# Kernel optimization log

Measured on AMD Instinct MI355X. Metric: run time of the kernel, lower is better.

## Reference

```python
import jax, jax.numpy as jnp
import numpy as np

B, A, N, K, F, E = 2, 5, 1000, 16, 256, 3


def setup_inputs() -> dict:
    key = jax.random.key(0)
    ks = jax.random.split(key, 6)
    nfeature = jax.random.normal(ks[0], (B, A, N, F), dtype=jnp.float32)
    nn_idx = jax.random.randint(ks[1], (B, A, N, K), 0, N)
    etype = jax.random.randint(ks[2], (B, A, N, K), 0, E)
    W = jax.random.normal(ks[3], (A, E, F, F), dtype=jnp.float32) * (1.0 / np.sqrt(F))
    b = jnp.zeros((A, E, F), dtype=jnp.float32)
    W1 = jax.random.normal(ks[4], (A, F, F), dtype=jnp.float32) * (1.0 / np.sqrt(F))
    W2 = jax.random.normal(ks[5], (A, F, F), dtype=jnp.float32) * (1.0 / np.sqrt(F))
    b2 = jnp.zeros((A, F), dtype=jnp.float32)
    return {"nfeature": nfeature, "nn_idx": nn_idx, "etype": etype,
            "W": W, "b": b, "W1": W1, "W2": W2, "b2": b2}


def reference(nfeature, nn_idx, etype, W, b, W1, W2, b2):
    Bs, As, Ns, Fs = nfeature.shape
    Ks = nn_idx.shape[-1]
    Es = W.shape[1]
    # gather neighbor features per anchor: [B, A, N, K, F]
    idx = nn_idx.reshape(Bs, As, Ns * Ks, 1)
    nbr = jnp.take_along_axis(nfeature, idx, axis=2).reshape(Bs, As, Ns, Ks, Fs)
    onehot = jax.nn.one_hot(etype, Es, dtype=nfeature.dtype)  # [B, A, N, K, E]
    # edge-type-specific pointwise transform (loop over small fixed E)
    msg = jnp.zeros((Bs, As, Ns, Ks, Fs), dtype=nfeature.dtype)
    for e in range(Es):
        y = jnp.einsum('bankf,afg->bankg', nbr, W[:, e]) + b[:, e][None, :, None, None, :]
        msg = msg + onehot[..., e:e + 1] * y
    pw = jax.nn.relu(msg.mean(axis=3))  # aggregate over K neighbors -> [B, A, N, F]
    # hop: mix each anchor with the summed 'mutual' feature
    mutual = pw.sum(axis=1)  # [B, N, F]
    hop = jax.nn.relu(jnp.einsum('banf,afg->bang', pw, W1)
                      + jnp.einsum('bnf,afg->bang', mutual, W2)
                      + b2[None, :, None, :])
    return hop + nfeature  # residual add
```

## Files before the change

### kernel.cpp

```cpp
#include <hip/hip_runtime.h>

typedef float f32x4 __attribute__((ext_vector_type(4)));
typedef __bf16 bf16x8 __attribute__((ext_vector_type(8)));
typedef unsigned short u16x4 __attribute__((ext_vector_type(4)));
typedef unsigned short u16x8 __attribute__((ext_vector_type(8)));

constexpr int B_ = 2, A_ = 5, N_ = 1000, K_ = 16, F_ = 256, E_ = 3;
constexpr int RTOT = B_ * N_;
constexpr int ROWS = 2016;
constexpr int TIL  = 32;
constexpr int NT   = ROWS / TIL;
constexpr int GBL  = NT * A_;
constexpr int KS1  = (E_ * F_) / 32;
constexpr int KS2  = (2 * F_) / 32;
constexpr int NTL  = F_ / 16;

constexpr int GATHER_BLOCKS = (A_ * ROWS) / 4;
constexpr int PACK_THREADS  = A_ * KS1 * NTL * 64 + A_ * KS2 * NTL * 64;
constexpr int PACK_BLOCKS   = PACK_THREADS / 256;

constexpr size_t SZ_WPK  = (size_t)A_ * KS1 * NTL * 512 * 2;
constexpr size_t OFF_W12 = SZ_WPK;
constexpr size_t SZ_W12  = (size_t)A_ * KS2 * NTL * 512 * 2;
constexpr size_t OFF_PWB = OFF_W12 + SZ_W12;
constexpr size_t SZ_PWB  = (size_t)A_ * ROWS * F_ * 2;
constexpr size_t OFF_SG  = OFF_PWB + SZ_PWB;
constexpr size_t SZ_SG   = (size_t)A_ * ROWS * (E_ * F_) * 2;
constexpr size_t OFF_CNT = OFF_SG + SZ_SG;

__device__ __forceinline__ unsigned short f2bf(float x) {
  unsigned int u = __builtin_bit_cast(unsigned int, x);
  u += 0x7fffu + ((u >> 16) & 1u);
  return (unsigned short)(u >> 16);
}
__device__ __forceinline__ float bf2f(unsigned short h) {
  return __builtin_bit_cast(float, (unsigned int)h << 16);
}
__device__ __forceinline__ int swz315(int bid) {
  const int xcd = bid & 7, idx = bid >> 3;
  return (xcd < 3 ? xcd * 40 : 120 + (xcd - 3) * 39) + idx;
}

__global__ __launch_bounds__(256) void k_gather_pack(
    const float* __restrict__ nf, const int* __restrict__ nn_idx,
    const int* __restrict__ et, const float* __restrict__ W,
    const float* __restrict__ W1, const float* __restrict__ W2,
    unsigned short* __restrict__ Sg, float* __restrict__ CNTS,
    unsigned short* __restrict__ wpk, unsigned short* __restrict__ w12)
{
  if (blockIdx.x < GATHER_BLOCKS) {
    const int bid  = blockIdx.x;
    const int nbid = (bid & 7) * (GATHER_BLOCKS / 8) + (bid >> 3);
    const int task = nbid * 4 + (threadIdx.x >> 6);
    const int lane = threadIdx.x & 63;
    const int a  = task / ROWS;
    const int rp = task - a * ROWS;
    const int rg = rp < RTOT ? rp : RTOT - 1;
    const int bb = rg / N_;
    const int n  = rg - bb * N_;
    const int eoff = ((bb * A_ + a) * N_ + n) * K_;

    int4 iv[4], ev[4];
#pragma unroll
    for (int q = 0; q < 4; ++q) {
      iv[q] = *reinterpret_cast<const int4*>(nn_idx + eoff + q * 4);
      ev[q] = *reinterpret_cast<const int4*>(et + eoff + q * 4);
    }
    const float* __restrict__ slab =
        nf + (size_t)(bb * A_ + a) * N_ * F_ + lane * 4;
    f32x4 a0 = {0.f, 0.f, 0.f, 0.f}, a1 = a0, a2 = a0;
    int c0 = 0, c1 = 0, c2 = 0;
#pragma unroll
    for (int q = 0; q < 4; ++q) {
#pragma unroll
      for (int j = 0; j < 4; ++j) {
        const int id = ((const int*)&iv[q])[j];
        const int e  = ((const int*)&ev[q])[j];
        const f32x4 v = *reinterpret_cast<const f32x4*>(slab + (size_t)id * F_);
        if (e == 0)      { a0 += v; ++c0; }
        else if (e == 1) { a1 += v; ++c1; }
        else             { a2 += v; ++c2; }
      }
    }
    unsigned short* __restrict__ row = Sg + ((size_t)a * ROWS + rp) * 768;
    const int sw = (rp & 7) << 3;
    u16x4 p0, p1, p2;
#pragma unroll
    for (int j = 0; j < 4; ++j) {
      p0[j] = f2bf(a0[j]); p1[j] = f2bf(a1[j]); p2[j] = f2bf(a2[j]);
    }
    *reinterpret_cast<u16x4*>(row + ((0 * F_ + lane * 4) ^ sw)) = p0;
    *reinterpret_cast<u16x4*>(row + ((1 * F_ + lane * 4) ^ sw)) = p1;
    *reinterpret_cast<u16x4*>(row + ((2 * F_ + lane * 4) ^ sw)) = p2;
    if (lane == 0) {
      f32x4 c = {(float)c0, (float)c1, (float)c2, 0.f};
      *reinterpret_cast<f32x4*>(CNTS + (size_t)task * 4) = c;
    }
  } else {
    const int id = (blockIdx.x - GATHER_BLOCKS) * 256 + threadIdx.x;
    const int T1 = A_ * KS1 * NTL * 64;
    const int T2 = A_ * KS2 * NTL * 64;
    if (id < T1) {
      const int lane = id & 63, nt = (id >> 6) & 15;
      const int r = id >> 10, t = r % KS1, a = r / KS1;
      const int k0 = t * 32 + (lane >> 4) * 8;
      const int n  = nt * 16 + (lane & 15);
      const float* src = W + ((size_t)a * E_ * F_ + k0) * F_ + n;
      u16x8 v;
#pragma unroll
      for (int j = 0; j < 8; ++j) v[j] = f2bf(src[(size_t)j * F_]);
      *reinterpret_cast<u16x8*>(wpk + (size_t)id * 8) = v;
    } else if (id < T1 + T2) {
      const int p = id - T1;
      const int lane = p & 63, nt = (p >> 6) & 15;
      const int r = p >> 10, t = r % KS2, a = r / KS2;
      const int k0 = t * 32 + (lane >> 4) * 8;
      const int n  = nt * 16 + (lane & 15);
      u16x8 v;
#pragma unroll
      for (int j = 0; j < 8; ++j) {
        const int k = k0 + j;
        const float s = (k < F_) ? W1[((size_t)a * F_ + k) * F_ + n]
                                 : W2[((size_t)a * F_ + (k - F_)) * F_ + n];
        v[j] = f2bf(s);
      }
      *reinterpret_cast<u16x8*>(w12 + (size_t)p * 8) = v;
    }
  }
}

__global__ __launch_bounds__(512) void k_gemm1(
    const unsigned short* __restrict__ Sg, const float* __restrict__ CNTS,
    const unsigned short* __restrict__ wpk, const float* __restrict__ bias,
    unsigned short* __restrict__ pwb)
{
  __shared__ alignas(16) unsigned short S[TIL * E_ * F_];
  __shared__ float CNT[TIL][4];
  const int lin = swz315(blockIdx.x);
  const int a   = lin / NT;
  const int r0  = (lin - a * NT) * TIL;
  const int tid = threadIdx.x;

  const unsigned short* src = Sg + ((size_t)a * ROWS + r0) * 768;
#pragma unroll
  for (int it = 0; it < 6; ++it) {
    const int off = (it * 512 + tid) * 8;
    __builtin_amdgcn_global_load_lds(
        (const __attribute__((address_space(1))) unsigned int*)(src + off),
        (__attribute__((address_space(3))) unsigned int*)(S + off), 16, 0, 0);
  }
  if (tid < TIL)
    *reinterpret_cast<f32x4*>(&CNT[tid][0]) =
        *reinterpret_cast<const f32x4*>(CNTS + (size_t)(a * ROWS + r0 + tid) * 4);
  __syncthreads();

  const int lane = tid & 63, wv = tid >> 6;
  const int arow = lane & 15, kg = lane >> 4;
  const unsigned short* __restrict__ Wp = wpk + (size_t)a * KS1 * NTL * 512;
  f32x4 acc[2][2];
#pragma unroll
  for (int c = 0; c < 2; ++c)
#pragma unroll
    for (int mb = 0; mb < 2; ++mb) acc[c][mb] = (f32x4){0.f, 0.f, 0.f, 0.f};
  const int ssw = (arow & 7) << 3;
#pragma unroll
  for (int t = 0; t < KS1; ++t) {
    bf16x8 af[2];
#pragma unroll
    for (int mb = 0; mb < 2; ++mb) {
      const int si = ((mb * 16 + arow) * 768 + t * 32 + kg * 8) ^ ssw;
      af[mb] = *reinterpret_cast<const bf16x8*>(&S[si]);
    }
#pragma unroll
    for (int c = 0; c < 2; ++c) {
      const int nt = wv * 2 + c;
      const bf16x8 bfr = *reinterpret_cast<const bf16x8*>(
          Wp + ((size_t)(t * NTL + nt) * 64 + lane) * 8);
#pragma unroll
      for (int mb = 0; mb < 2; ++mb)
        acc[c][mb] = __builtin_amdgcn_mfma_f32_16x16x32_bf16(af[mb], bfr, acc[c][mb], 0, 0, 0);
    }
  }

  const float* __restrict__ ba = bias + a * E_ * F_;
#pragma unroll
  for (int c = 0; c < 2; ++c) {
    const int col = (wv * 2 + c) * 16 + arow;
    const float b0 = ba[col], b1 = ba[F_ + col], b2v = ba[2 * F_ + col];
#pragma unroll
    for (int mb = 0; mb < 2; ++mb) {
#pragma unroll
      for (int rr = 0; rr < 4; ++rr) {
        const int row = mb * 16 + kg * 4 + rr;
        const int r   = r0 + row;
        float x = (acc[c][mb][rr] + CNT[row][0] * b0 + CNT[row][1] * b1 +
                   CNT[row][2] * b2v) * (1.0f / K_);
        x = fmaxf(x, 0.f);
        pwb[((size_t)a * ROWS + r) * F_ + (col ^ ((row & 7) << 3))] = f2bf(x);
      }
    }
  }
}

__global__ __launch_bounds__(512) void k_hop_mfma(
    const unsigned short* __restrict__ pwb, const unsigned short* __restrict__ w12,
    const float* __restrict__ b2, const float* __restrict__ nf,
    float* __restrict__ out)
{
  __shared__ alignas(16) unsigned short S2[2 * TIL * F_];
  const int lin = swz315(blockIdx.x);
  const int a   = lin / NT;
  const int r0  = (lin - a * NT) * TIL;
  const int tid = threadIdx.x;

  const unsigned short* srcP = pwb + ((size_t)a * ROWS + r0) * F_;
#pragma unroll
  for (int it = 0; it < 2; ++it) {
    const int off = (it * 512 + tid) * 8;
    __builtin_amdgcn_global_load_lds(
        (const __attribute__((address_space(1))) unsigned int*)(srcP + off),
        (__attribute__((address_space(3))) unsigned int*)(S2 + off), 16, 0, 0);
  }
#pragma unroll
  for (int it = 0; it < 2; ++it) {
    const int i = (it * 512 + tid) * 8;
    float s[8] = {0.f, 0.f, 0.f, 0.f, 0.f, 0.f, 0.f, 0.f};
#pragma unroll
    for (int a2 = 0; a2 < A_; ++a2) {
      const u16x8 v = *reinterpret_cast<const u16x8*>(
          pwb + ((size_t)a2 * ROWS + r0) * F_ + i);
#pragma unroll
      for (int j = 0; j < 8; ++j) s[j] += bf2f(v[j]);
    }
    u16x8 o;
#pragma unroll
    for (int j = 0; j < 8; ++j) o[j] = f2bf(s[j]);
    *reinterpret_cast<u16x8*>(&S2[TIL * F_ + i]) = o;
  }
  __syncthreads();

  const int lane = tid & 63, wv = tid >> 6;
  const int arow = lane & 15, kg = lane >> 4;
  const unsigned short* __restrict__ Wp = w12 + (size_t)a * KS2 * NTL * 512;
  f32x4 acc[2][2];
#pragma unroll
  for (int c = 0; c < 2; ++c)
#pragma unroll
    for (int mb = 0; mb < 2; ++mb) acc[c][mb] = (f32x4){0.f, 0.f, 0.f, 0.f};
  const int ssw = (arow & 7) << 3;
#pragma unroll
  for (int t = 0; t < KS2; ++t) {
    const int half = t >> 3;
    const int kk   = (t & 7) * 32;
    bf16x8 af[2];
#pragma unroll
    for (int mb = 0; mb < 2; ++mb) {
      const int si = half * (TIL * F_) + (mb * 16 + arow) * F_ + ((kk + kg * 8) ^ ssw);
      af[mb] = *reinterpret_cast<const bf16x8*>(&S2[si]);
    }
#pragma unroll
    for (int c = 0; c < 2; ++c) {
      const int nt = wv * 2 + c;
      const bf16x8 bfr = *reinterpret_cast<const bf16x8*>(
          Wp + ((size_t)(t * NTL + nt) * 64 + lane) * 8);
#pragma unroll
      for (int mb = 0; mb < 2; ++mb)
        acc[c][mb] = __builtin_amdgcn_mfma_f32_16x16x32_bf16(af[mb], bfr, acc[c][mb], 0, 0, 0);
    }
  }

#pragma unroll
  for (int c = 0; c < 2; ++c) {
    const int col = (wv * 2 + c) * 16 + arow;
    const float bb2 = b2[a * F_ + col];
#pragma unroll
    for (int mb = 0; mb < 2; ++mb) {
#pragma unroll
      for (int rr = 0; rr < 4; ++rr) {
        const int row = mb * 16 + kg * 4 + rr;
        const int r   = r0 + row;
        if (r < RTOT) {
          const int bb = r / N_, n = r - bb * N_;
          const size_t o = ((size_t)(bb * A_ + a) * N_ + n) * F_ + col;
          out[o] = fmaxf(acc[c][mb][rr] + bb2, 0.f) + nf[o];
        }
      }
    }
  }
}

extern "C" void kernel_launch(void* const* d_in, const int* in_sizes, int n_in,
                              void* d_out, int out_size, void* d_ws, size_t ws_size,
                              hipStream_t stream)
{
  const float* nf     = (const float*)d_in[0];
  const int*   nn_idx = (const int*)  d_in[1];
  const int*   et     = (const int*)  d_in[2];
  const float* W      = (const float*)d_in[3];
  const float* bias   = (const float*)d_in[4];
  const float* W1     = (const float*)d_in[5];
  const float* W2     = (const float*)d_in[6];
  const float* b2     = (const float*)d_in[7];
  float* out = (float*)d_out;

  unsigned short* wpk  = (unsigned short*)d_ws;
  unsigned short* w12  = (unsigned short*)((char*)d_ws + OFF_W12);
  unsigned short* pwb  = (unsigned short*)((char*)d_ws + OFF_PWB);
  unsigned short* Sg   = (unsigned short*)((char*)d_ws + OFF_SG);
  float*          CNTS = (float*)((char*)d_ws + OFF_CNT);

  k_gather_pack<<<dim3(GATHER_BLOCKS + PACK_BLOCKS), 256, 0, stream>>>(
      nf, nn_idx, et, W, W1, W2, Sg, CNTS, wpk, w12);

  k_gemm1<<<dim3(GBL), 512, 0, stream>>>(Sg, CNTS, wpk, bias, pwb);
  k_hop_mfma<<<dim3(GBL), 512, 0, stream>>>(pwb, w12, b2, nf, out);
}
```

Before: 47.97 us.

## Fuse neighbor gather into first GEMM via shared memory, split weight packing

The gather-and-bucket step now writes its per-edge-type sums straight into shared memory inside the first GEMM kernel, using 16-row tiles of 256 threads. This removes the global round trip of the bf16 gathered buffer and the count buffer. Weight packing moves into its own small kernel that runs before the fused kernel, which now waits for it. The risks are less reuse of each weight fragment per block, because tiles are smaller, and a serial pack launch on the critical path.

```diff
diff --git a/kernel.cpp b/kernel.cpp
--- a/kernel.cpp
+++ b/kernel.cpp
@@ -8,25 +8,24 @@
 constexpr int B_ = 2, A_ = 5, N_ = 1000, K_ = 16, F_ = 256, E_ = 3;
 constexpr int RTOT = B_ * N_;
 constexpr int ROWS = 2016;
-constexpr int TIL  = 32;
-constexpr int NT   = ROWS / TIL;
-constexpr int GBL  = NT * A_;
+constexpr int TILE = 16;
+constexpr int NT1  = RTOT / TILE;
+constexpr int GBL1 = NT1 * A_;
+constexpr int TIL2 = 32;
+constexpr int NT2  = ROWS / TIL2;
+constexpr int GBL2 = NT2 * A_;
 constexpr int KS1  = (E_ * F_) / 32;
 constexpr int KS2  = (2 * F_) / 32;
 constexpr int NTL  = F_ / 16;
 
-constexpr int GATHER_BLOCKS = (A_ * ROWS) / 4;
-constexpr int PACK_THREADS  = A_ * KS1 * NTL * 64 + A_ * KS2 * NTL * 64;
-constexpr int PACK_BLOCKS   = PACK_THREADS / 256;
+constexpr int PACK_THREADS = A_ * KS1 * NTL * 64 + A_ * KS2 * NTL * 64;
+constexpr int PACK_BLOCKS  = PACK_THREADS / 256;
 
 constexpr size_t SZ_WPK  = (size_t)A_ * KS1 * NTL * 512 * 2;
 constexpr size_t OFF_W12 = SZ_WPK;
 constexpr size_t SZ_W12  = (size_t)A_ * KS2 * NTL * 512 * 2;
 constexpr size_t OFF_PWB = OFF_W12 + SZ_W12;
 constexpr size_t SZ_PWB  = (size_t)A_ * ROWS * F_ * 2;
-constexpr size_t OFF_SG  = OFF_PWB + SZ_PWB;
-constexpr size_t SZ_SG   = (size_t)A_ * ROWS * (E_ * F_) * 2;
-constexpr size_t OFF_CNT = OFF_SG + SZ_SG;
 
 __device__ __forceinline__ unsigned short f2bf(float x) {
   unsigned int u = __builtin_bit_cast(unsigned int, x);
@@ -36,30 +35,70 @@
 __device__ __forceinline__ float bf2f(unsigned short h) {
   return __builtin_bit_cast(float, (unsigned int)h << 16);
 }
+__device__ __forceinline__ int swz625(int bid) {
+  const int xcd = bid & 7, idx = bid >> 3;
+  return (xcd == 0 ? 0 : 79 + (xcd - 1) * 78) + idx;
+}
 __device__ __forceinline__ int swz315(int bid) {
   const int xcd = bid & 7, idx = bid >> 3;
   return (xcd < 3 ? xcd * 40 : 120 + (xcd - 3) * 39) + idx;
 }
 
-__global__ __launch_bounds__(256) void k_gather_pack(
+__global__ __launch_bounds__(256) void k_pack(
+    const float* __restrict__ W, const float* __restrict__ W1,
+    const float* __restrict__ W2, unsigned short* __restrict__ wpk,
+    unsigned short* __restrict__ w12)
+{
+  const int id = blockIdx.x * 256 + threadIdx.x;
+  const int T1 = A_ * KS1 * NTL * 64;
+  const int T2 = A_ * KS2 * NTL * 64;
+  if (id < T1) {
+    const int lane = id & 63, nt = (id >> 6) & 15;
+    const int r = id >> 10, t = r % KS1, a = r / KS1;
+    const int k0 = t * 32 + (lane >> 4) * 8;
+    const int n  = nt * 16 + (lane & 15);
+    const float* src = W + ((size_t)a * E_ * F_ + k0) * F_ + n;
+    u16x8 v;
+#pragma unroll
+    for (int j = 0; j < 8; ++j) v[j] = f2bf(src[(size_t)j * F_]);
+    *reinterpret_cast<u16x8*>(wpk + (size_t)id * 8) = v;
+  } else if (id < T1 + T2) {
+    const int p = id - T1;
+    const int lane = p & 63, nt = (p >> 6) & 15;
+    const int r = p >> 10, t = r % KS2, a = r / KS2;
+    const int k0 = t * 32 + (lane >> 4) * 8;
+    const int n  = nt * 16 + (lane & 15);
+    u16x8 v;
+#pragma unroll
+    for (int j = 0; j < 8; ++j) {
+      const int k = k0 + j;
+      const float s = (k < F_) ? W1[((size_t)a * F_ + k) * F_ + n]
+                               : W2[((size_t)a * F_ + (k - F_)) * F_ + n];
+      v[j] = f2bf(s);
+    }
+    *reinterpret_cast<u16x8*>(w12 + (size_t)p * 8) = v;
+  }
+}
+
+__global__ __launch_bounds__(256) void k_fused(
     const float* __restrict__ nf, const int* __restrict__ nn_idx,
-    const int* __restrict__ et, const float* __restrict__ W,
-    const float* __restrict__ W1, const float* __restrict__ W2,
-    unsigned short* __restrict__ Sg, float* __restrict__ CNTS,
-    unsigned short* __restrict__ wpk, unsigned short* __restrict__ w12)
-{
-  if (blockIdx.x < GATHER_BLOCKS) {
-    const int bid  = blockIdx.x;
-    const int nbid = (bid & 7) * (GATHER_BLOCKS / 8) + (bid >> 3);
-    const int task = nbid * 4 + (threadIdx.x >> 6);
-    const int lane = threadIdx.x & 63;
-    const int a  = task / ROWS;
-    const int rp = task - a * ROWS;
-    const int rg = rp < RTOT ? rp : RTOT - 1;
-    const int bb = rg / N_;
-    const int n  = rg - bb * N_;
+    const int* __restrict__ et, const unsigned short* __restrict__ wpk,
+    const float* __restrict__ bias, unsigned short* __restrict__ pwb)
+{
+  __shared__ alignas(16) unsigned short S[TILE * E_ * F_];
+  __shared__ float CNT[TILE][4];
+  const int lin = swz625(blockIdx.x);
+  const int a   = lin / NT1;
+  const int r0  = (lin - a * NT1) * TILE;
+  const int tid = threadIdx.x;
+  const int lane = tid & 63, wv = tid >> 6;
+
+#pragma unroll
+  for (int rr = 0; rr < 4; ++rr) {
+    const int row = wv * 4 + rr;
+    const int r   = r0 + row;
+    const int bb  = r / N_, n = r - bb * N_;
     const int eoff = ((bb * A_ + a) * N_ + n) * K_;
-
     int4 iv[4], ev[4];
 #pragma unroll
     for (int q = 0; q < 4; ++q) {
@@ -82,122 +121,53 @@
         else             { a2 += v; ++c2; }
       }
     }
-    unsigned short* __restrict__ row = Sg + ((size_t)a * ROWS + rp) * 768;
-    const int sw = (rp & 7) << 3;
+    const int sw = (row & 7) << 3;
     u16x4 p0, p1, p2;
 #pragma unroll
     for (int j = 0; j < 4; ++j) {
       p0[j] = f2bf(a0[j]); p1[j] = f2bf(a1[j]); p2[j] = f2bf(a2[j]);
     }
-    *reinterpret_cast<u16x4*>(row + ((0 * F_ + lane * 4) ^ sw)) = p0;
-    *reinterpret_cast<u16x4*>(row + ((1 * F_ + lane * 4) ^ sw)) = p1;
-    *reinterpret_cast<u16x4*>(row + ((2 * F_ + lane * 4) ^ sw)) = p2;
+    *reinterpret_cast<u16x4*>(&S[(row * 768 + 0 * F_ + lane * 4) ^ sw]) = p0;
+    *reinterpret_cast<u16x4*>(&S[(row * 768 + 1 * F_ + lane * 4) ^ sw]) = p1;
+    *reinterpret_cast<u16x4*>(&S[(row * 768 + 2 * F_ + lane * 4) ^ sw]) = p2;
     if (lane == 0) {
-      f32x4 c = {(float)c0, (float)c1, (float)c2, 0.f};
-      *reinterpret_cast<f32x4*>(CNTS + (size_t)task * 4) = c;
-    }
-  } else {
-    const int id = (blockIdx.x - GATHER_BLOCKS) * 256 + threadIdx.x;
-    const int T1 = A_ * KS1 * NTL * 64;
-    const int T2 = A_ * KS2 * NTL * 64;
-    if (id < T1) {
-      const int lane = id & 63, nt = (id >> 6) & 15;
-      const int r = id >> 10, t = r % KS1, a = r / KS1;
-      const int k0 = t * 32 + (lane >> 4) * 8;
-      const int n  = nt * 16 + (lane & 15);
-      const float* src = W + ((size_t)a * E_ * F_ + k0) * F_ + n;
-      u16x8 v;
-#pragma unroll
-      for (int j = 0; j < 8; ++j) v[j] = f2bf(src[(size_t)j * F_]);
-      *reinterpret_cast<u16x8*>(wpk + (size_t)id * 8) = v;
-    } else if (id < T1 + T2) {
-      const int p = id - T1;
-      const int lane = p & 63, nt = (p >> 6) & 15;
-      const int r = p >> 10, t = r % KS2, a = r / KS2;
-      const int k0 = t * 32 + (lane >> 4) * 8;
-      const int n  = nt * 16 + (lane & 15);
-      u16x8 v;
-#pragma unroll
-      for (int j = 0; j < 8; ++j) {
-        const int k = k0 + j;
-        const float s = (k < F_) ? W1[((size_t)a * F_ + k) * F_ + n]
-                                 : W2[((size_t)a * F_ + (k - F_)) * F_ + n];
-        v[j] = f2bf(s);
-      }
-      *reinterpret_cast<u16x8*>(w12 + (size_t)p * 8) = v;
-    }
-  }
-}
-
-__global__ __launch_bounds__(512) void k_gemm1(
-    const unsigned short* __restrict__ Sg, const float* __restrict__ CNTS,
-    const unsigned short* __restrict__ wpk, const float* __restrict__ bias,
-    unsigned short* __restrict__ pwb)
-{
-  __shared__ alignas(16) unsigned short S[TIL * E_ * F_];
-  __shared__ float CNT[TIL][4];
-  const int lin = swz315(blockIdx.x);
-  const int a   = lin / NT;
-  const int r0  = (lin - a * NT) * TIL;
-  const int tid = threadIdx.x;
-
-  const unsigned short* src = Sg + ((size_t)a * ROWS + r0) * 768;
-#pragma unroll
-  for (int it = 0; it < 6; ++it) {
-    const int off = (it * 512 + tid) * 8;
-    __builtin_amdgcn_global_load_lds(
-        (const __attribute__((address_space(1))) unsigned int*)(src + off),
-        (__attribute__((address_space(3))) unsigned int*)(S + off), 16, 0, 0);
-  }
-  if (tid < TIL)
-    *reinterpret_cast<f32x4*>(&CNT[tid][0]) =
-        *reinterpret_cast<const f32x4*>(CNTS + (size_t)(a * ROWS + r0 + tid) * 4);
+      CNT[row][0] = (float)c0; CNT[row][1] = (float)c1; CNT[row][2] = (float)c2;
+    }
+  }
   __syncthreads();
 
-  const int lane = tid & 63, wv = tid >> 6;
   const int arow = lane & 15, kg = lane >> 4;
   const unsigned short* __restrict__ Wp = wpk + (size_t)a * KS1 * NTL * 512;
-  f32x4 acc[2][2];
-#pragma unroll
-  for (int c = 0; c < 2; ++c)
-#pragma unroll
-    for (int mb = 0; mb < 2; ++mb) acc[c][mb] = (f32x4){0.f, 0.f, 0.f, 0.f};
+  f32x4 acc[4];
+#pragma unroll
+  for (int m = 0; m < 4; ++m) acc[m] = (f32x4){0.f, 0.f, 0.f, 0.f};
   const int ssw = (arow & 7) << 3;
 #pragma unroll
   for (int t = 0; t < KS1; ++t) {
-    bf16x8 af[2];
-#pragma unroll
-    for (int mb = 0; mb < 2; ++mb) {
-      const int si = ((mb * 16 + arow) * 768 + t * 32 + kg * 8) ^ ssw;
-      af[mb] = *reinterpret_cast<const bf16x8*>(&S[si]);
-    }
-#pragma unroll
-    for (int c = 0; c < 2; ++c) {
-      const int nt = wv * 2 + c;
+    const int si = (arow * 768 + t * 32 + kg * 8) ^ ssw;
+    const bf16x8 af = *reinterpret_cast<const bf16x8*>(&S[si]);
+#pragma unroll
+    for (int m = 0; m < 4; ++m) {
+      const int nt = wv * 4 + m;
       const bf16x8 bfr = *reinterpret_cast<const bf16x8*>(
           Wp + ((size_t)(t * NTL + nt) * 64 + lane) * 8);
-#pragma unroll
-      for (int mb = 0; mb < 2; ++mb)
-        acc[c][mb] = __builtin_amdgcn_mfma_f32_16x16x32_bf16(af[mb], bfr, acc[c][mb], 0, 0, 0);
+      acc[m] = __builtin_amdgcn_mfma_f32_16x16x32_bf16(af, bfr, acc[m], 0, 0, 0);
     }
   }
 
   const float* __restrict__ ba = bias + a * E_ * F_;
 #pragma unroll
-  for (int c = 0; c < 2; ++c) {
-    const int col = (wv * 2 + c) * 16 + arow;
+  for (int m = 0; m < 4; ++m) {
+    const int col = (wv * 4 + m) * 16 + arow;
     const float b0 = ba[col], b1 = ba[F_ + col], b2v = ba[2 * F_ + col];
 #pragma unroll
-    for (int mb = 0; mb < 2; ++mb) {
-#pragma unroll
-      for (int rr = 0; rr < 4; ++rr) {
-        const int row = mb * 16 + kg * 4 + rr;
-        const int r   = r0 + row;
-        float x = (acc[c][mb][rr] + CNT[row][0] * b0 + CNT[row][1] * b1 +
-                   CNT[row][2] * b2v) * (1.0f / K_);
-        x = fmaxf(x, 0.f);
-        pwb[((size_t)a * ROWS + r) * F_ + (col ^ ((row & 7) << 3))] = f2bf(x);
-      }
+    for (int rr = 0; rr < 4; ++rr) {
+      const int row = kg * 4 + rr;
+      const int r   = r0 + row;
+      float x = (acc[m][rr] + CNT[row][0] * b0 + CNT[row][1] * b1 +
+                 CNT[row][2] * b2v) * (1.0f / K_);
+      x = fmaxf(x, 0.f);
+      pwb[((size_t)a * ROWS + r) * F_ + (col ^ ((row & 7) << 3))] = f2bf(x);
     }
   }
 }
@@ -207,10 +177,10 @@
     const float* __restrict__ b2, const float* __restrict__ nf,
     float* __restrict__ out)
 {
-  __shared__ alignas(16) unsigned short S2[2 * TIL * F_];
+  __shared__ alignas(16) unsigned short S2[2 * TIL2 * F_];
   const int lin = swz315(blockIdx.x);
-  const int a   = lin / NT;
-  const int r0  = (lin - a * NT) * TIL;
+  const int a   = lin / NT2;
+  const int r0  = (lin - a * NT2) * TIL2;
   const int tid = threadIdx.x;
 
   const unsigned short* srcP = pwb + ((size_t)a * ROWS + r0) * F_;
@@ -235,7 +205,7 @@
     u16x8 o;
 #pragma unroll
     for (int j = 0; j < 8; ++j) o[j] = f2bf(s[j]);
-    *reinterpret_cast<u16x8*>(&S2[TIL * F_ + i]) = o;
+    *reinterpret_cast<u16x8*>(&S2[TIL2 * F_ + i]) = o;
   }
   __syncthreads();
 
@@ -255,7 +225,7 @@
     bf16x8 af[2];
 #pragma unroll
     for (int mb = 0; mb < 2; ++mb) {
-      const int si = half * (TIL * F_) + (mb * 16 + arow) * F_ + ((kk + kg * 8) ^ ssw);
+      const int si = half * (TIL2 * F_) + (mb * 16 + arow) * F_ + ((kk + kg * 8) ^ ssw);
       af[mb] = *reinterpret_cast<const bf16x8*>(&S2[si]);
     }
 #pragma unroll
@@ -303,15 +273,11 @@
   const float* b2     = (const float*)d_in[7];
   float* out = (float*)d_out;
 
-  unsigned short* wpk  = (unsigned short*)d_ws;
-  unsigned short* w12  = (unsigned short*)((char*)d_ws + OFF_W12);
-  unsigned short* pwb  = (unsigned short*)((char*)d_ws + OFF_PWB);
-  unsigned short* Sg   = (unsigned short*)((char*)d_ws + OFF_SG);
-  float*          CNTS = (float*)((char*)d_ws + OFF_CNT);
-
-  k_gather_pack<<<dim3(GATHER_BLOCKS + PACK_BLOCKS), 256, 0, stream>>>(
-      nf, nn_idx, et, W, W1, W2, Sg, CNTS, wpk, w12);
-
-  k_gemm1<<<dim3(GBL), 512, 0, stream>>>(Sg, CNTS, wpk, bias, pwb);
-  k_hop_mfma<<<dim3(GBL), 512, 0, stream>>>(pwb, w12, b2, nf, out);
-}
+  unsigned short* wpk = (unsigned short*)d_ws;
+  unsigned short* w12 = (unsigned short*)((char*)d_ws + OFF_W12);
+  unsigned short* pwb = (unsigned short*)((char*)d_ws + OFF_PWB);
+
+  k_pack<<<dim3(PACK_BLOCKS), 256, 0, stream>>>(W, W1, W2, wpk, w12);
+  k_fused<<<dim3(GBL1), 256, 0, stream>>>(nf, nn_idx, et, wpk, bias, pwb);
+  k_hop_mfma<<<dim3(GBL2), 512, 0, stream>>>(pwb, w12, b2, nf, out);
+}
```

Result: slower. 56.27 us (+17.3%).
